# Kernel tuning notes

Measured on AMD Instinct MI355X. Metric: run time of the kernel, lower is better.

## Reference

```python
import jax, jax.numpy as jnp
import numpy as np

NUM_RAYS = 524288
NUM_EXISTING = 64   # coarse samples per ray
NUM_SAMPLES = 64    # fine PDF samples -> num_bins = 65
HIST_PAD = 0.01
EPS = 1e-5


def setup_inputs() -> dict:
    key = jax.random.key(0)
    kw, kd = jax.random.split(key)
    weights = jax.random.uniform(kw, (NUM_RAYS, NUM_EXISTING, 1), dtype=jnp.float32)
    # build monotonically increasing per-ray bin edges (near plane ~2.0)
    deltas = jax.random.uniform(kd, (NUM_RAYS, NUM_EXISTING + 1), dtype=jnp.float32,
                                minval=0.01, maxval=0.1)
    edges = 2.0 + jnp.cumsum(deltas, axis=-1)          # [R, N+1]
    starts = edges[..., :-1, None]                      # [R, N, 1]
    ends = edges[..., 1:, None]                         # [R, N, 1]
    return {"weights": weights, "starts": starts, "ends": ends}


def _pdf_sample(weights, starts, ends):
    # weights/starts/ends: [R, N, 1]
    w = weights[..., 0] + HIST_PAD                      # [R, N]
    ws = jnp.sum(w, axis=-1, keepdims=True)             # [R, 1]
    padding = jax.nn.relu(EPS - ws)
    w = w + padding / w.shape[-1]
    ws = ws + padding
    pdf = w / ws
    cdf = jnp.minimum(jnp.ones_like(pdf), jnp.cumsum(pdf, axis=-1))
    cdf = jnp.concatenate([jnp.zeros_like(cdf[..., :1]), cdf], axis=-1)  # [R, N+1]

    num_bins = NUM_SAMPLES + 1
    u = jnp.linspace(0.0, 1.0, num_bins, dtype=cdf.dtype)
    u = jnp.broadcast_to(u, (*cdf.shape[:-1], num_bins))                 # [R, num_bins]

    s = starts[..., 0]
    e = ends[..., 0]
    existing_bins = jnp.concatenate(
        [s[..., :1], (s[..., 1:] + e[..., :-1]) / 2.0, e[..., -1:]], axis=-1)  # [R, N+1]

    inds = jax.vmap(lambda c, uu: jnp.searchsorted(c, uu, side='right'))(cdf, u)
    nmax = existing_bins.shape[-1] - 1
    below = jnp.clip(inds - 1, 0, nmax)
    above = jnp.clip(inds, 0, nmax)
    cdf_g0 = jnp.take_along_axis(cdf, below, axis=-1)
    bins_g0 = jnp.take_along_axis(existing_bins, below, axis=-1)
    cdf_g1 = jnp.take_along_axis(cdf, above, axis=-1)
    bins_g1 = jnp.take_along_axis(existing_bins, above, axis=-1)

    t = jnp.clip(jnp.nan_to_num((u - cdf_g0) / (cdf_g1 - cdf_g0), nan=0.0), 0.0, 1.0)
    bins = bins_g0 + t * (bins_g1 - bins_g0)             # [R, num_bins]
    # include_original=True: merge with existing bins and sort
    bins = jnp.sort(jnp.concatenate([existing_bins, bins], axis=-1), axis=-1)  # [R, 2N+2]
    return bins


def reference(weights, starts, ends):
    bins = _pdf_sample(weights, starts, ends)
    # bin_starts = bins[..., :-1, None], bin_ends = bins[..., 1:, None]
    return bins
```

## Files before the change

kernel.cpp:

```cpp
#include <hip/hip_runtime.h>


#define NUM_RAYS 524288
#define NE 64
#define HIST_PAD 0.01f
#define EPS_PAD 1e-5f

constexpr int WAVES = 4;
constexpr int RPW   = 4;
constexpr int RPB   = WAVES * RPW;
constexpr int BLOCK = WAVES * 64;
constexpr int ROW   = 130;

template <int CTRL, int ROW_MASK = 0xf>
__device__ __forceinline__ float dpp0f(float x) {
    return __int_as_float(
        __builtin_amdgcn_update_dpp(0, __float_as_int(x), CTRL, ROW_MASK, 0xf, true));
}

__global__ __launch_bounds__(BLOCK) void pdf_sample_kernel(
    const float* __restrict__ weights,
    const float* __restrict__ starts,
    const float* __restrict__ ends,
    float* __restrict__ out)
{
    __shared__ __align__(16) float s_o[RPB][ROW];

    const int lane = threadIdx.x & 63;
    const int wvid = threadIdx.x >> 6;
    const int ray0 = blockIdx.x * RPB + wvid * RPW;

    float wl[RPW], sl[RPW], el[RPW];
    #pragma unroll
    for (int r = 0; r < RPW; ++r) {
        const unsigned ib = (unsigned)(ray0 + r) * NE;
        wl[r] = weights[ib + lane];
        sl[r] = starts [ib + lane];
        el[r] = ends   [ib + 63];
    }

    #pragma unroll
    for (int r = 0; r < RPW; ++r) {
        const int   row    = wvid * RPW + r;
        const float w      = wl[r] + HIST_PAD;
        const float s      = sl[r];
        const float e_last = el[r];

        float c = w;
        c += dpp0f<0x111>(c);
        c += dpp0f<0x112>(c);
        c += dpp0f<0x114>(c);
        c += dpp0f<0x118>(c);
        c += dpp0f<0x142, 0xa>(c);
        c += dpp0f<0x143, 0xc>(c);

        const float ws      = __int_as_float(__builtin_amdgcn_readlane(__float_as_int(c), 63));
        const float padding = fmaxf(EPS_PAD - ws, 0.0f);
        float rtot;
        asm("v_rcp_f32 %0, %1" : "=v"(rtot) : "v"(ws + padding));
        const float pad64 = padding * (1.0f / 64.0f);

        const float cdfk = fminf(fmaf((float)(lane + 1), pad64, c) * rtot, 1.0f);
        const int   tcur = (int)ceilf(cdfk * 64.0f);

        const float c0p   = dpp0f<0x138>(cdfk);
        const int   tprev = (int)ceilf(c0p * 64.0f);
        float b1n = dpp0f<0x130>(s);
        if (lane == 63) b1n = e_last;

        s_o[row][lane + tprev] = s;

        const float denom = cdfk - c0p;
        float rden;
        asm("v_rcp_f32 %0, %1" : "=v"(rden) : "v"(denom));
        const float slope = (b1n - s) * rden;
        float v = fmaf((float)tprev, 1.0f / 64.0f, -c0p);
        for (int j = tprev; j < tcur; ++j) {
            s_o[row][j + lane + 1] = fmaf(v, slope, s);
            v += 1.0f / 64.0f;
        }

        if (lane == 63) {
            s_o[row][2 * NE + 1] = e_last;
            s_o[row][NE + tcur]  = e_last;
            for (int j = tcur; j < NE; ++j)
                s_o[row][j + NE + 1] = e_last;
        }
    }

    __syncthreads();

    const float4* sf = (const float4*)&s_o[0][0];
    float4* ob = (float4*)(out + (size_t)blockIdx.x * (RPB * ROW));
    const int t = threadIdx.x;
    ob[t]         = sf[t];
    ob[t + BLOCK] = sf[t + BLOCK];
    if (t < RPB * ROW / 4 - 2 * BLOCK)
        ob[t + 2 * BLOCK] = sf[t + 2 * BLOCK];
}

extern "C" void kernel_launch(void* const* d_in, const int* in_sizes, int n_in,
                              void* d_out, int out_size, void* d_ws, size_t ws_size,
                              hipStream_t stream) {
    const float* weights = (const float*)d_in[0];
    const float* starts  = (const float*)d_in[1];
    const float* ends    = (const float*)d_in[2];
    float* out = (float*)d_out;

    const int grid = NUM_RAYS / RPB;
    pdf_sample_kernel<<<grid, BLOCK, 0, stream>>>(weights, starts, ends, out);
}
```

Before: 112.7 us.

## Use per-wave output staging, double rays per wave, pack end loads

Each wave now owns its own slice of shared memory and writes it out directly once its LDS writes drain, which removes the block-wide barrier. Rays per wave go from 4 to 8, so shared memory per block doubles and more work is amortized per wave. The per-ray end values are fetched with one packed load and then taken via readlane, replacing one redundant load per ray. The cost is higher register and LDS use, which may reduce occupancy, and correctness now depends on the wave-local lgkmcnt wait.

```diff
diff --git a/kernel.cpp b/kernel.cpp
--- a/kernel.cpp
+++ b/kernel.cpp
@@ -7,7 +7,7 @@
 #define EPS_PAD 1e-5f
 
 constexpr int WAVES = 4;
-constexpr int RPW   = 4;
+constexpr int RPW   = 8;
 constexpr int RPB   = WAVES * RPW;
 constexpr int BLOCK = WAVES * 64;
 constexpr int ROW   = 130;
@@ -30,21 +30,25 @@
     const int wvid = threadIdx.x >> 6;
     const int ray0 = blockIdx.x * RPB + wvid * RPW;
 
-    float wl[RPW], sl[RPW], el[RPW];
+    const float e_pack = ends[(unsigned)(ray0 + (lane & 7)) * NE + 63u];
+
+    float wl[RPW], sl[RPW];
     #pragma unroll
     for (int r = 0; r < RPW; ++r) {
-        const unsigned ib = (unsigned)(ray0 + r) * NE;
-        wl[r] = weights[ib + lane];
-        sl[r] = starts [ib + lane];
-        el[r] = ends   [ib + 63];
+        const unsigned ib = (unsigned)(ray0 + r) * NE + (unsigned)lane;
+        wl[r] = weights[ib];
+        sl[r] = starts [ib];
     }
+
+    float* const srow_base = &s_o[wvid * RPW][0];
 
     #pragma unroll
     for (int r = 0; r < RPW; ++r) {
-        const int   row    = wvid * RPW + r;
+        float* const srow = srow_base + r * ROW;
         const float w      = wl[r] + HIST_PAD;
         const float s      = sl[r];
-        const float e_last = el[r];
+        const float e_last = __int_as_float(
+            __builtin_amdgcn_readlane(__float_as_int(e_pack), r));
 
         float c = w;
         c += dpp0f<0x111>(c);
@@ -68,7 +72,7 @@
         float b1n = dpp0f<0x130>(s);
         if (lane == 63) b1n = e_last;
 
-        s_o[row][lane + tprev] = s;
+        srow[lane + tprev] = s;
 
         const float denom = cdfk - c0p;
         float rden;
@@ -76,27 +80,27 @@
         const float slope = (b1n - s) * rden;
         float v = fmaf((float)tprev, 1.0f / 64.0f, -c0p);
         for (int j = tprev; j < tcur; ++j) {
-            s_o[row][j + lane + 1] = fmaf(v, slope, s);
+            srow[j + lane + 1] = fmaf(v, slope, s);
             v += 1.0f / 64.0f;
         }
 
         if (lane == 63) {
-            s_o[row][2 * NE + 1] = e_last;
-            s_o[row][NE + tcur]  = e_last;
+            srow[2 * NE + 1] = e_last;
+            srow[NE + tcur]  = e_last;
             for (int j = tcur; j < NE; ++j)
-                s_o[row][j + NE + 1] = e_last;
+                srow[j + NE + 1] = e_last;
         }
     }
 
-    __syncthreads();
+    asm volatile("s_waitcnt lgkmcnt(0)" ::: "memory");
 
-    const float4* sf = (const float4*)&s_o[0][0];
-    float4* ob = (float4*)(out + (size_t)blockIdx.x * (RPB * ROW));
-    const int t = threadIdx.x;
-    ob[t]         = sf[t];
-    ob[t + BLOCK] = sf[t + BLOCK];
-    if (t < RPB * ROW / 4 - 2 * BLOCK)
-        ob[t + 2 * BLOCK] = sf[t + 2 * BLOCK];
+    const float4* sf = (const float4*)srow_base;
+    float4* ob = (float4*)(out + (size_t)ray0 * ROW);
+    #pragma unroll
+    for (int k = 0; k < 4; ++k)
+        ob[lane + k * 64] = sf[lane + k * 64];
+    if (lane < 4)
+        ob[lane + 256] = sf[lane + 256];
 }
 
 extern "C" void kernel_launch(void* const* d_in, const int* in_sizes, int n_in,
```

Result: no change. 114.2 us (+1.3%).
